# Optimization experiments

Measured on AMD Instinct MI355X. Metric: run time of the kernel, lower is better.

The kernel has to match this reference:

```python
import jax, jax.numpy as jnp
import numpy as np


def setup_inputs() -> dict:
    key = jax.random.key(0)
    k1, k2, k3, k4 = jax.random.split(key, 4)
    B, F, E, A = 2048, 50, 64, 64  # batch, field_dim, embedding_dim, attention_size
    return {
        "inputs": jax.random.normal(k1, (B, F, E), dtype=jnp.float32),
        "weight_attention": jax.random.normal(k2, (E, A), dtype=jnp.float32) * 0.05,
        "weight_projection": jax.random.normal(k3, (A,), dtype=jnp.float32) * 0.05,
        "weight_bias": jax.random.normal(k4, (1, A), dtype=jnp.float32) * 0.05,
    }


def reference(inputs, weight_attention, weight_projection, weight_bias):
    # inputs: [B, F, E]
    F = inputs.shape[1]
    idx_i, idx_j = jnp.triu_indices(F, k=1)  # P = F*(F-1)/2 pairs
    # Pairwise element-wise products: [B, P, E]
    ewp = inputs[:, idx_i, :] * inputs[:, idx_j, :]
    # Small attention MLP: [B, P, A]
    att = jnp.einsum('bpe,ea->bpa', ewp, weight_attention)
    relu = jax.nn.relu(att + weight_bias)  # bias broadcasts [1, A]
    score = jnp.sum(weight_projection * relu, axis=2, keepdims=True)  # [B, P, 1]
    # Faithful to TF source: tf.nn.softmax default axis=-1 over a size-1 axis
    att_out = jax.nn.softmax(score, axis=-1)
    # Weighted sum pooling over pairs: [B, E]
    afm = jnp.sum(att_out * ewp, axis=1)
    return afm
```

## Files before the change

### kernel.cpp

```cpp
#include <hip/hip_runtime.h>


template <int F>
__global__ __launch_bounds__(256) void afm_sum_kernel(const float* __restrict__ x,
                                                      float* __restrict__ out,
                                                      int B, int E) {
    const int ecols = E >> 1;
    const int total = B * ecols;
    int tid = blockIdx.x * blockDim.x + threadIdx.x;
    if (tid >= total) return;
    int b = tid / ecols;
    int c = tid - b * ecols;

    const float2* xp = reinterpret_cast<const float2*>(x) + (size_t)b * F * ecols + c;

    float2 s  = make_float2(0.f, 0.f);
    float2 ss = make_float2(0.f, 0.f);
#pragma unroll
    for (int f = 0; f < F; ++f) {
        float2 v = xp[(size_t)f * ecols];
        s.x += v.x;
        s.y += v.y;
        ss.x = fmaf(v.x, v.x, ss.x);
        ss.y = fmaf(v.y, v.y, ss.y);
    }

    float2 o;
    o.x = 0.5f * (s.x * s.x - ss.x);
    o.y = 0.5f * (s.y * s.y - ss.y);
    reinterpret_cast<float2*>(out)[tid] = o;
}

__global__ __launch_bounds__(256) void afm_sum_generic(const float* __restrict__ x,
                                                       float* __restrict__ out,
                                                       int B, int E, int F) {
    const int ecols = E >> 1;
    const int total = B * ecols;
    int tid = blockIdx.x * blockDim.x + threadIdx.x;
    if (tid >= total) return;
    int b = tid / ecols;
    int c = tid - b * ecols;

    const float2* xp = reinterpret_cast<const float2*>(x) + (size_t)b * F * ecols + c;

    float2 s  = make_float2(0.f, 0.f);
    float2 ss = make_float2(0.f, 0.f);
#pragma unroll 10
    for (int f = 0; f < F; ++f) {
        float2 v = xp[(size_t)f * ecols];
        s.x += v.x;
        s.y += v.y;
        ss.x = fmaf(v.x, v.x, ss.x);
        ss.y = fmaf(v.y, v.y, ss.y);
    }

    float2 o;
    o.x = 0.5f * (s.x * s.x - ss.x);
    o.y = 0.5f * (s.y * s.y - ss.y);
    reinterpret_cast<float2*>(out)[tid] = o;
}

extern "C" void kernel_launch(void* const* d_in, const int* in_sizes, int n_in,
                              void* d_out, int out_size, void* d_ws, size_t ws_size,
                              hipStream_t stream) {
    const float* x = (const float*)d_in[0];
    float* out = (float*)d_out;

    const int A = in_sizes[2];
    const int E = in_sizes[1] / A;
    const int B = out_size / E;
    const int F = in_sizes[0] / (B * E);

    const int total = B * (E >> 1);
    const int block = 256;
    const int grid = (total + block - 1) / block;

    if (F == 50) {
        afm_sum_kernel<50><<<grid, block, 0, stream>>>(x, out, B, E);
    } else {
        afm_sum_generic<<<grid, block, 0, stream>>>(x, out, B, E, F);
    }
}
```

Before: 9.377 us.

## Assign one wavefront per batch row with float4 loads and shuffle reduction

The specialised kernel now gives each 64-lane wavefront one batch row. Lanes split into 16 float4 columns by 4 field slices, and the partial sum and sum-of-squares are combined with xor shuffles. This cuts the serial 50-load chain per thread down to about 13 wider loads and doubles the thread count, so more memory requests are in flight. The cost is shuffle work, a tail branch for the leftover two fields, and a hardcoded F=50, E=64 fast path.

```diff
diff --git a/kernel.cpp b/kernel.cpp
--- a/kernel.cpp
+++ b/kernel.cpp
@@ -1,34 +1,59 @@
 #include <hip/hip_runtime.h>
 
 
-template <int F>
-__global__ __launch_bounds__(256) void afm_sum_kernel(const float* __restrict__ x,
-                                                      float* __restrict__ out,
-                                                      int B, int E) {
-    const int ecols = E >> 1;
-    const int total = B * ecols;
-    int tid = blockIdx.x * blockDim.x + threadIdx.x;
-    if (tid >= total) return;
-    int b = tid / ecols;
-    int c = tid - b * ecols;
+__global__ __launch_bounds__(256) void afm_wave_kernel(const float* __restrict__ x,
+                                                       float* __restrict__ out,
+                                                       int B) {
+    constexpr int F = 50;
+    constexpr int C4 = 16;
+    const int wid = threadIdx.x >> 6;
+    const int lane = threadIdx.x & 63;
+    const int b = blockIdx.x * 4 + wid;
+    if (b >= B) return;
 
-    const float2* xp = reinterpret_cast<const float2*>(x) + (size_t)b * F * ecols + c;
+    const int c4 = lane & 15;
+    const int fs = lane >> 4;
 
-    float2 s  = make_float2(0.f, 0.f);
-    float2 ss = make_float2(0.f, 0.f);
+    const float4* xb = reinterpret_cast<const float4*>(x) + (size_t)b * F * C4;
+    const float4* xp = xb + fs * C4 + c4;
+
+    float4 s  = make_float4(0.f, 0.f, 0.f, 0.f);
+    float4 ss = make_float4(0.f, 0.f, 0.f, 0.f);
+
 #pragma unroll
-    for (int f = 0; f < F; ++f) {
-        float2 v = xp[(size_t)f * ecols];
-        s.x += v.x;
-        s.y += v.y;
+    for (int k = 0; k < 12; ++k) {
+        float4 v = xp[k * 4 * C4];
+        s.x += v.x; s.y += v.y; s.z += v.z; s.w += v.w;
         ss.x = fmaf(v.x, v.x, ss.x);
         ss.y = fmaf(v.y, v.y, ss.y);
+        ss.z = fmaf(v.z, v.z, ss.z);
+        ss.w = fmaf(v.w, v.w, ss.w);
+    }
+    if (fs < 2) {
+        float4 v = xb[(48 + fs) * C4 + c4];
+        s.x += v.x; s.y += v.y; s.z += v.z; s.w += v.w;
+        ss.x = fmaf(v.x, v.x, ss.x);
+        ss.y = fmaf(v.y, v.y, ss.y);
+        ss.z = fmaf(v.z, v.z, ss.z);
+        ss.w = fmaf(v.w, v.w, ss.w);
     }
 
-    float2 o;
-    o.x = 0.5f * (s.x * s.x - ss.x);
-    o.y = 0.5f * (s.y * s.y - ss.y);
-    reinterpret_cast<float2*>(out)[tid] = o;
+#pragma unroll
+    for (int m = 16; m <= 32; m <<= 1) {
+        s.x += __shfl_xor(s.x, m);  s.y += __shfl_xor(s.y, m);
+        s.z += __shfl_xor(s.z, m);  s.w += __shfl_xor(s.w, m);
+        ss.x += __shfl_xor(ss.x, m); ss.y += __shfl_xor(ss.y, m);
+        ss.z += __shfl_xor(ss.z, m); ss.w += __shfl_xor(ss.w, m);
+    }
+
+    if (fs == 0) {
+        float4 o;
+        o.x = 0.5f * (s.x * s.x - ss.x);
+        o.y = 0.5f * (s.y * s.y - ss.y);
+        o.z = 0.5f * (s.z * s.z - ss.z);
+        o.w = 0.5f * (s.w * s.w - ss.w);
+        reinterpret_cast<float4*>(out)[(size_t)b * C4 + c4] = o;
+    }
 }
 
 __global__ __launch_bounds__(256) void afm_sum_generic(const float* __restrict__ x,
@@ -71,13 +96,14 @@
     const int B = out_size / E;
     const int F = in_sizes[0] / (B * E);
 
-    const int total = B * (E >> 1);
-    const int block = 256;
-    const int grid = (total + block - 1) / block;
-
-    if (F == 50) {
-        afm_sum_kernel<50><<<grid, block, 0, stream>>>(x, out, B, E);
+    if (F == 50 && E == 64) {
+        const int block = 256;
+        const int grid = (B + 3) / 4;
+        afm_wave_kernel<<<grid, block, 0, stream>>>(x, out, B);
     } else {
+        const int total = B * (E >> 1);
+        const int block = 256;
+        const int grid = (total + block - 1) / block;
         afm_sum_generic<<<grid, block, 0, stream>>>(x, out, B, E, F);
     }
 }
```

Result: slower. 9.730 us (+3.8%).
